# Kernel tuning notes

Measured on AMD Instinct MI355X. Metric: run time of the kernel, lower is better.

Reference implementation:

```python
import jax, jax.numpy as jnp
import numpy as np

B, N, IN, E, OUT = 4, 128, 256, 128, 128
EPS = 1e-5
NEG = -1.0e9


def _ln(x, s, o):
    m = x.mean(-1, keepdims=True)
    v = ((x - m) ** 2).mean(-1, keepdims=True)
    return s * jax.lax.rsqrt(v + EPS) * (x - m) + o


def setup_inputs() -> dict:
    key = jax.random.key(0)
    ks = jax.random.split(key, 30)

    def w(k, i, o):
        return (jax.random.normal(k, (i, o), jnp.float32) / np.sqrt(i)).astype(jnp.float32)

    z_dense = jax.random.normal(ks[0], (B, N, IN), jnp.float32)
    e_dense = jax.random.normal(ks[1], (B, N, N, E), jnp.float32)
    graph_fts = jax.random.normal(ks[2], (B, IN // 2), jnp.float32)
    lengths = jax.random.randint(ks[3], (B,), N // 2, N + 1)
    mask = jnp.arange(N)[None, :] < lengths[:, None]  # (B,N) bool
    adj = jax.random.uniform(ks[4], (B, N, N)) < 0.3
    adj = (adj | jnp.eye(N, dtype=bool)[None]) & mask[:, :, None] & mask[:, None, :]
    return dict(
        z_dense=z_dense, e_dense=e_dense, graph_fts=graph_fts, mask=mask, adj_mat=adj,
        Wt1=w(ks[5], IN, 8), Wt2=w(ks[6], IN, 8), Wt3=w(ks[7], IN, 8),
        We1=w(ks[8], E, 8), We2=w(ks[9], E, 8), We3=w(ks[10], E, 8),
        Wg=w(ks[11], IN // 2, 8),
        Wm1=w(ks[12], IN, OUT), Wm2=w(ks[13], IN, OUT), Wme=w(ks[14], E, OUT), Wmg=w(ks[15], E, OUT),
        ln1_s=jnp.ones((OUT,), jnp.float32), ln1_o=jnp.zeros((OUT,), jnp.float32),
        Wmlp1=w(ks[16], OUT, OUT),
        ln2_s=jnp.ones((OUT,), jnp.float32), ln2_o=jnp.zeros((OUT,), jnp.float32),
        Wmlp2=w(ks[17], OUT, OUT),
        WU1=w(ks[18], IN, OUT), WU2=w(ks[19], OUT, OUT), WU3=w(ks[20], 8, OUT),
        lnf_s=jnp.ones((OUT,), jnp.float32), lnf_o=jnp.zeros((OUT,), jnp.float32),
    )


def reference(z_dense, e_dense, graph_fts, mask, adj_mat,
              Wt1, Wt2, Wt3, We1, We2, We3, Wg,
              Wm1, Wm2, Wme, Wmg,
              ln1_s, ln1_o, Wmlp1, ln2_s, ln2_o, Wmlp2,
              WU1, WU2, WU3, lnf_s, lnf_o):
    mN = mask[..., None]  # (B,N,1)
    # --- triplet messages ---
    tri_1 = jnp.where(mN, z_dense @ Wt1, 0.0)  # (B,N,8)
    tri_2 = jnp.where(mN, z_dense @ Wt2, 0.0)
    tri_3 = jnp.where(mN, z_dense @ Wt3, 0.0)
    tri_e1 = e_dense @ We1  # (B,N,N,8)
    tri_e2 = e_dense @ We2
    tri_e3 = e_dense @ We3
    tri_g = graph_fts @ Wg  # (B,8)
    # (B,N,N,N,8) 7-way broadcast sum (axes: b, i, j, k)
    tri = (tri_1[:, :, None, None, :] + tri_2[:, None, :, None, :] + tri_3[:, None, None, :, :]
           + tri_e1[:, :, :, None, :] + tri_e2[:, :, None, :, :] + tri_e3[:, None, :, :, :]
           + tri_g[:, None, None, None, :])
    msk_tri = mask[:, None, None, :] | mask[:, None, :, None] | mask[:, :, None, None]
    tri = jnp.where(msk_tri[..., None], tri, NEG)
    tri_pooled = tri.max(axis=1)  # (B,N,N,8) -- max over first node axis
    tri_msgs = jax.nn.relu(tri_pooled @ WU3)  # (B,N,N,OUT)

    # --- pairwise messages ---
    msg_1 = jnp.where(mN, z_dense @ Wm1, 0.0)  # (B,N,OUT)
    msg_2 = jnp.where(mN, z_dense @ Wm2, 0.0)
    msg_e = jnp.where(adj_mat[..., None], e_dense @ Wme, 0.0)  # (B,N,N,OUT)
    msg_g = graph_fts @ Wmg  # (B,OUT)
    msgs = msg_1[:, None, :, :] + msg_2[:, :, None, :] + msg_e + msg_g[:, None, None, :]
    # M[-1]: [LN, ReLU, Linear] x2
    x = jax.nn.relu(_ln(msgs, ln1_s, ln1_o)) @ Wmlp1
    x = jax.nn.relu(_ln(x, ln2_s, ln2_o)) @ Wmlp2
    msgs = jnp.where(adj_mat[..., None], x, NEG).max(axis=1)  # (B,N,OUT)

    ret = _ln(z_dense @ WU1 + msgs @ WU2, lnf_s, lnf_o)  # (B,N,OUT)
    return ret, msgs, tri_msgs
```

## Files before the change

### kernel.cpp

```cpp
#include <hip/hip_runtime.h>

#define BN   4
#define NN   128
#define INF  256
#define EF   128
#define OUTF 128
#define EPSF 1e-5f
#define NEGF -998244352.0f

typedef __attribute__((ext_vector_type(8))) short short8;
typedef __attribute__((ext_vector_type(4))) float f32x4;

#define MFMA16(a, b, c) __builtin_amdgcn_mfma_f32_16x16x32_bf16(a, b, c, 0, 0, 0)

__device__ __forceinline__ unsigned short f2bf(float f) {
    unsigned u = __float_as_uint(f);
    u += 0x7fffu + ((u >> 16) & 1u);
    return (unsigned short)(u >> 16);
}
__device__ __forceinline__ unsigned pack2(float a, float b) {
    return (unsigned)f2bf(a) | ((unsigned)f2bf(b) << 16);
}

constexpr size_t TRI1 = 0;
constexpr size_t TRI2 = 4096;
constexpr size_t TRI3 = 8192;
constexpr size_t MSG1 = 12288;
constexpr size_t MSG2 = 77824;
constexpr size_t ZWU1 = 143360;
constexpr size_t TRIG = 208896;
constexpr size_t MSGG = 209920;
constexpr size_t E1T  = 210944;
constexpr size_t E2T  = 735232;
constexpr size_t E3N  = 1259520;
constexpr size_t PREPF = 1914880;

constexpr int W1T_OFF  = 0;
constexpr int W2T_OFF  = 16384;
constexpr int WMET_OFF = 32768;

constexpr size_t O_RET = 0;
constexpr size_t O_MSG = 65536;
constexpr size_t O_TRI = 131072;

__device__ __forceinline__ int detect_int(const void* mask) {
    const unsigned char* m = (const unsigned char*)mask;
    return (m[1] | m[2] | m[3]) == 0 ? 1 : 0;
}
__device__ __forceinline__ bool rdbool(const void* p, size_t idx, int isInt) {
    if (isInt) return ((const int*)p)[idx] != 0;
    return ((const unsigned char*)p)[idx] != 0;
}

__device__ __forceinline__ void stage_h(const unsigned short* __restrict__ prep, int offU,
                                        unsigned short* Wl, int w, int lane)
{
    const char* g = (const char*)(prep + offU) + w * 4096 + lane * 16;
    char* l = (char*)Wl + w * 4096;
    #pragma unroll
    for (int r = 0; r < 4; r++) {
        __builtin_amdgcn_global_load_lds(
            (const __attribute__((address_space(1))) void*)(g + r * 1024),
            (__attribute__((address_space(3))) void*)(l + r * 1024),
            16, 0, 0);
    }
}

__global__ __launch_bounds__(256, 4) void k_pre(
    const float* __restrict__ z, const float* __restrict__ e, const void* __restrict__ mask,
    const float* __restrict__ Wt1, const float* __restrict__ Wt2, const float* __restrict__ Wt3,
    const float* __restrict__ Wm1, const float* __restrict__ Wm2, const float* __restrict__ WU1,
    const float* __restrict__ g, const float* __restrict__ Wg, const float* __restrict__ Wmg,
    const float* __restrict__ W1, const float* __restrict__ W2, const float* __restrict__ Wme,
    const float* __restrict__ We1, const float* __restrict__ We2, const float* __restrict__ We3,
    float* __restrict__ ws, unsigned short* __restrict__ prep)
{
    int bx = blockIdx.x, tid = threadIdx.x;
    __shared__ __align__(16) unsigned char smem[128 * 136 * 2];

    if (bx < 512) {
        unsigned short* Ab = (unsigned short*)smem;
        int bi = bx;
        int b = bi >> 7, i = bi & 127;
        int lane = tid & 63, w = tid >> 6, q = lane >> 4, n = lane & 15;
        {
            int half = lane >> 5, c4 = (lane & 31) * 4;
            #pragma unroll
            for (int it = 0; it < 16; it++) {
                int row = 32 * w + 2 * it + half;
                float4 v = *(const float4*)(e + (size_t)bi * 16384 + (size_t)row * 128 + c4);
                unsigned* dst = (unsigned*)&Ab[row * 136 + c4];
                dst[0] = pack2(v.x, v.y);
                dst[1] = pack2(v.z, v.w);
            }
        }
        float t1v;
        {
            int c = lane & 7, kk = lane >> 3;
            const float* zr = z + (size_t)bi * INF;
            float s = 0.f;
            #pragma unroll
            for (int m = 0; m < 32; m++) s = fmaf(zr[kk * 32 + m], Wt1[(kk * 32 + m) * 8 + c], s);
            s += __shfl_xor(s, 8, 64);
            s += __shfl_xor(s, 16, 64);
            s += __shfl_xor(s, 32, 64);
            int isInt = detect_int(mask);
            t1v = rdbool(mask, bi, isInt) ? s : 0.f;
        }
        short8 bfrag[4][2];
        {
            #pragma unroll
            for (int t = 0; t < 2; t++) {
                int col = 16 * t + n;
                const float* Wsel = (col < 8) ? We1 : (col < 16 ? We2 : We3);
                int csel = col & 7;
                float mval = (col < 24) ? 1.f : 0.f;
                #pragma unroll
                for (int ks = 0; ks < 4; ks++) {
                    union { short8 s; unsigned short u[8]; } tmp;
                    #pragma unroll
                    for (int jj = 0; jj < 8; jj++) {
                        int k = ks * 32 + q * 8 + jj;
                        tmp.u[jj] = f2bf(Wsel[k * 8 + csel] * mval);
                    }
                    bfrag[ks][t] = tmp.s;
                }
            }
        }
        __builtin_amdgcn_wave_barrier();

        f32x4 ac2[2][2];
        #pragma unroll
        for (int rt = 0; rt < 2; rt++)
            #pragma unroll
            for (int t = 0; t < 2; t++) ac2[rt][t] = 0.f;
        #pragma unroll
        for (int ks = 0; ks < 4; ks++) {
            int k0 = ks * 32 + q * 8;
            short8 a0 = *(const short8*)&Ab[(32 * w + n) * 136 + k0];
            short8 a1 = *(const short8*)&Ab[(32 * w + 16 + n) * 136 + k0];
            #pragma unroll
            for (int t = 0; t < 2; t++) {
                ac2[0][t] = MFMA16(a0, bfrag[ks][t], ac2[0][t]);
                ac2[1][t] = MFMA16(a1, bfrag[ks][t], ac2[1][t]);
            }
        }
        #pragma unroll
        for (int rt = 0; rt < 2; rt++)
            #pragma unroll
            for (int reg = 0; reg < 4; reg++) {
                int row = 32 * w + 16 * rt + 4 * q + reg;
                float v0 = ac2[rt][0][reg];
                if (n < 8) ws[E1T + ((size_t)(b * 128 + row) * 128 + i) * 8 + n] = v0 + t1v;
                else       ws[E2T + ((size_t)(b * 128 + row) * 128 + i) * 8 + (n - 8)] = v0;
                if (n < 8) ws[E3N + ((size_t)bi * 128 + row) * 8 + n] = ac2[rt][1][reg];
            }
        return;
    }
    if (bx < 1024) {
        int bn = bx - 512;
        int isInt = detect_int(mask);
        float* zr = (float*)smem;
        zr[tid] = z[(size_t)bn * INF + tid];
        __syncthreads();
        float mk = rdbool(mask, bn, isInt) ? 1.f : 0.f;
        for (int idx = tid; idx < 408; idx += 256) {
            const float* W; int c; size_t dst; int width; bool msk;
            if (idx < 8)        { W = Wt1; c = idx;       dst = TRI1 + (size_t)bn * 8;   width = 8;   msk = true;  }
            else if (idx < 16)  { W = Wt2; c = idx - 8;   dst = TRI2 + (size_t)bn * 8;   width = 8;   msk = true;  }
            else if (idx < 24)  { W = Wt3; c = idx - 16;  dst = TRI3 + (size_t)bn * 8;   width = 8;   msk = true;  }
            else if (idx < 152) { W = Wm1; c = idx - 24;  dst = MSG1 + (size_t)bn * 128; width = 128; msk = true;  }
            else if (idx < 280) { W = Wm2; c = idx - 152; dst = MSG2 + (size_t)bn * 128; width = 128; msk = true;  }
            else                { W = WU1; c = idx - 280; dst = ZWU1 + (size_t)bn * 128; width = 128; msk = false; }
            float a0 = 0.f, a1 = 0.f;
            #pragma unroll 8
            for (int k = 0; k < INF; k += 2) {
                a0 += zr[k] * W[k * width + c];
                a1 += zr[k + 1] * W[(k + 1) * width + c];
            }
            float acc = a0 + a1;
            ws[dst + c] = msk ? acc * mk : acc;
        }
        return;
    }
    if (bx < 1028) {
        int b = bx - 1024;
        float* gr = (float*)smem;
        if (tid < 128) gr[tid] = g[b * 128 + tid];
        __syncthreads();
        if (tid < 8) {
            float a = 0.f;
            for (int k = 0; k < 128; k++) a += gr[k] * Wg[k * 8 + tid];
            ws[TRIG + b * 8 + tid] = a;
        } else if (tid >= 128) {
            int c = tid - 128;
            float a = 0.f;
            for (int k = 0; k < 128; k++) a += gr[k] * Wmg[k * 128 + c];
            ws[MSGG + b * 128 + c] = a;
        }
        return;
    }
    {
        int idx = (bx - 1028) * 256 + tid;
        const float* W = (idx < 16384) ? W1 : (idx < 32768 ? W2 : Wme);
        int local = idx & 16383;
        int f = local >> 3, jj = local & 7;
        int lane = f & 63, fg = f >> 6;
        int t = fg & 7, ks = fg >> 3;
        int n = lane & 15, q = lane >> 4;
        int row = 16 * t + n;
        int k = ks * 32 + q * 8 + jj;
        prep[idx] = f2bf(W[k * 128 + row]);
    }
}

#define PAIR_GEMM_H(HS) do {                                                   \
    _Pragma("unroll")                                                          \
    for (int ls = 0; ls < 2; ls++) {                                           \
        int kf = (2 * (HS) + ls) * 32 + q * 8;                                 \
        short8 a0 = *(const short8*)&Ab[(32 * w + n) * 136 + kf];              \
        short8 a1 = *(const short8*)&Ab[(32 * w + 16 + n) * 136 + kf];         \
        _Pragma("unroll")                                                      \
        for (int t = 0; t < 8; t++) {                                          \
            short8 bt = *(const short8*)&Wl[((ls * 8 + t) * 64 + lane) * 8];   \
            acc[0][t] = MFMA16(a0, bt, acc[0][t]);                             \
            acc[1][t] = MFMA16(a1, bt, acc[1][t]);                             \
        }                                                                      \
    }                                                                          \
} while (0)

__global__ __launch_bounds__(256, 3) void k_main(
    const float* __restrict__ e, const void* __restrict__ mask, const void* __restrict__ adj,
    const float* __restrict__ ln1s, const float* __restrict__ ln1o,
    const float* __restrict__ ln2s, const float* __restrict__ ln2o,
    const unsigned short* __restrict__ prep, const float* __restrict__ WU3,
    const float* __restrict__ WU2, const float* __restrict__ lnfs, const float* __restrict__ lnfo,
    float* __restrict__ ws, float* __restrict__ out)
{
    int bx = blockIdx.x, tid = threadIdx.x;
    __shared__ __align__(16) unsigned char smem[53248];
    int lane = tid & 63, w = tid >> 6, q = lane >> 4, n = lane & 15;
    int isInt = detect_int(mask);

    if (bx < 256) {
        int g = bx;
        int j0 = ((g >> 3) & 7) * 16, k0 = (g & 7) * 16, b = g >> 6;
        int wi = w >> 1, wc = w & 1;
        int tj = lane >> 3, tk = lane & 7;
        int col4 = (tid & 31) * 4, rowgrp = tid >> 5;

        int lenb;
        {
            unsigned long long m0 = __ballot(rdbool(mask, (size_t)b * 128 + lane, isInt));
            unsigned long long m1 = __ballot(rdbool(mask, (size_t)b * 128 + 64 + lane, isInt));
            lenb = __popcll(m0) + __popcll(m1);
        }
        bool needU = (j0 + 15 >= lenb) && (k0 + 15 >= lenb);

        float* Pb = (float*)smem + w * 1152;
        float* Qb = Pb + 576;

        f32x4 aM[2][2];
        #pragma unroll
        for (int jj = 0; jj < 2; jj++)
            #pragma unroll
            for (int kk = 0; kk < 2; kk++) aM[jj][kk] = NEGF;

        if (!needU) {
            for (int ch = 0; ch < 8; ch++) {
                int ibase = wi * 64 + ch * 8;
                #pragma unroll
                for (int r = 0; r < 2; r++) {
                    int f = r * 64 + lane;
                    int jr = f >> 3, ii = f & 7;
                    f32x4 pv = *(const f32x4*)(ws + E1T + (size_t)(b * 128 + j0 + jr) * 1024 + (ibase + ii) * 8 + wc * 4);
                    f32x4 qv = *(const f32x4*)(ws + E2T + (size_t)(b * 128 + k0 + jr) * 1024 + (ibase + ii) * 8 + wc * 4);
                    *(f32x4*)(Pb + jr * 36 + ii * 4) = pv;
                    *(f32x4*)(Qb + jr * 36 + ii * 4) = qv;
                }
                __builtin_amdgcn_wave_barrier();
                #pragma unroll
                for (int ii = 0; ii < 8; ii++) {
                    f32x4 p0 = *(const f32x4*)(Pb + tj * 36 + ii * 4);
                    f32x4 p1 = *(const f32x4*)(Pb + (tj + 8) * 36 + ii * 4);
                    f32x4 q0 = *(const f32x4*)(Qb + tk * 36 + ii * 4);
                    f32x4 q1 = *(const f32x4*)(Qb + (tk + 8) * 36 + ii * 4);
                    aM[0][0] = __builtin_elementwise_max(aM[0][0], p0 + q0);
                    aM[0][1] = __builtin_elementwise_max(aM[0][1], p0 + q1);
                    aM[1][0] = __builtin_elementwise_max(aM[1][0], p1 + q0);
                    aM[1][1] = __builtin_elementwise_max(aM[1][1], p1 + q1);
                }
            }
        } else {
            f32x4 aU[2][2];
            #pragma unroll
            for (int jj = 0; jj < 2; jj++)
                #pragma unroll
                for (int kk = 0; kk < 2; kk++) aU[jj][kk] = NEGF;
            unsigned long long mball = __ballot(rdbool(mask, (size_t)b * 128 + wi * 64 + lane, isInt));
            for (int ch = 0; ch < 8; ch++) {
                int ibase = wi * 64 + ch * 8;
                #pragma unroll
                for (int r = 0; r < 2; r++) {
                    int f = r * 64 + lane;
                    int jr = f >> 3, ii = f & 7;
                    f32x4 pv = *(const f32x4*)(ws + E1T + (size_t)(b * 128 + j0 + jr) * 1024 + (ibase + ii) * 8 + wc * 4);
                    f32x4 qv = *(const f32x4*)(ws + E2T + (size_t)(b * 128 + k0 + jr) * 1024 + (ibase + ii) * 8 + wc * 4);
                    *(f32x4*)(Pb + jr * 36 + ii * 4) = pv;
                    *(f32x4*)(Qb + jr * 36 + ii * 4) = qv;
                }
                __builtin_amdgcn_wave_barrier();
                #pragma unroll
                for (int ii = 0; ii < 8; ii++) {
                    f32x4 p0 = *(const f32x4*)(Pb + tj * 36 + ii * 4);
                    f32x4 p1 = *(const f32x4*)(Pb + (tj + 8) * 36 + ii * 4);
                    f32x4 q0 = *(const f32x4*)(Qb + tk * 36 + ii * 4);
                    f32x4 q1 = *(const f32x4*)(Qb + (tk + 8) * 36 + ii * 4);
                    f32x4 v00 = p0 + q0, v01 = p0 + q1, v10 = p1 + q0, v11 = p1 + q1;
                    if ((mball >> (ch * 8 + ii)) & 1) {
                        aM[0][0] = __builtin_elementwise_max(aM[0][0], v00);
                        aM[0][1] = __builtin_elementwise_max(aM[0][1], v01);
                        aM[1][0] = __builtin_elementwise_max(aM[1][0], v10);
                        aM[1][1] = __builtin_elementwise_max(aM[1][1], v11);
                    } else {
                        aU[0][0] = __builtin_elementwise_max(aU[0][0], v00);
                        aU[0][1] = __builtin_elementwise_max(aU[0][1], v01);
                        aU[1][0] = __builtin_elementwise_max(aU[1][0], v10);
                        aU[1][1] = __builtin_elementwise_max(aU[1][1], v11);
                    }
                }
            }
            bool mj[2], mk2[2];
            mj[0]  = (j0 + tj)     < lenb;
            mj[1]  = (j0 + tj + 8) < lenb;
            mk2[0] = (k0 + tk)     < lenb;
            mk2[1] = (k0 + tk + 8) < lenb;
            #pragma unroll
            for (int jj = 0; jj < 2; jj++)
                #pragma unroll
                for (int kk = 0; kk < 2; kk++)
                    if (mj[jj] | mk2[kk])
                        aM[jj][kk] = __builtin_elementwise_max(aM[jj][kk], aU[jj][kk]);
        }
        __syncthreads();
        float* pooled = (float*)smem;
        float4 wvr[8];
        #pragma unroll
        for (int c = 0; c < 8; c++) wvr[c] = *(const float4*)(WU3 + c * 128 + col4);

        if (wi == 0) {
            #pragma unroll
            for (int jj = 0; jj < 2; jj++)
                #pragma unroll
                for (int kk = 0; kk < 2; kk++) {
                    int p = (tj + 8 * jj) * 16 + (tk + 8 * kk);
                    #pragma unroll
                    for (int cc = 0; cc < 4; cc++)
                        pooled[(wc * 4 + cc) * 260 + p] = aM[jj][kk][cc];
                }
        }
        __syncthreads();
        if (wi == 1) {
            const float* tg = ws + TRIG + (size_t)b * 8 + wc * 4;
            #pragma unroll
            for (int jj = 0; jj < 2; jj++)
                #pragma unroll
                for (int kk = 0; kk < 2; kk++) {
                    int jv = j0 + tj + 8 * jj, kv = k0 + tk + 8 * kk;
                    const float* t2 = ws + TRI2 + (size_t)(b * 128 + jv) * 8 + wc * 4;
                    const float* t3 = ws + TRI3 + (size_t)(b * 128 + kv) * 8 + wc * 4;
                    const float* e3 = ws + E3N + ((size_t)(b * 128 + jv) * 128 + kv) * 8 + wc * 4;
                    int p = (tj + 8 * jj) * 16 + (tk + 8 * kk);
                    #pragma unroll
                    for (int cc = 0; cc < 4; cc++) {
                        int idx = (wc * 4 + cc) * 260 + p;
                        pooled[idx] = fmaxf(pooled[idx], aM[jj][kk][cc]) + t2[cc] + t3[cc] + e3[cc] + tg[cc];
                    }
                }
        }
        __syncthreads();
        #pragma unroll
        for (int pass = 0; pass < 32; pass++) {
            int p = pass * 8 + rowgrp;
            float4 s = { 0.f, 0.f, 0.f, 0.f };
            #pragma unroll
            for (int c = 0; c < 8; c++) {
                float pv = pooled[c * 260 + p];
                s.x += pv * wvr[c].x; s.y += pv * wvr[c].y;
                s.z += pv * wvr[c].z; s.w += pv * wvr[c].w;
            }
            s.x = fmaxf(s.x, 0.f); s.y = fmaxf(s.y, 0.f);
            s.z = fmaxf(s.z, 0.f); s.w = fmaxf(s.w, 0.f);
            int pj = p >> 4, pk = p & 15;
            *(float4*)(out + O_TRI + ((size_t)(b * 128 + j0 + pj) * 128 + (k0 + pk)) * 128 + col4) = s;
        }
        return;
    }

    unsigned short* Ab = (unsigned short*)smem;
    float* pw = (float*)(smem + 34816);
    unsigned short* Wl = (unsigned short*)(smem + 36864);
    float* mrowL = (float*)(smem + 36864);
    float* partL = mrowL + 128;
    float* redL  = partL + 256;
    int bj = bx - 256;
    int b = bj >> 7, j = bj & 127;

    int lenb;
    {
        unsigned long long m0 = __ballot(rdbool(mask, (size_t)b * 128 + lane, isInt));
        unsigned long long m1 = __ballot(rdbool(mask, (size_t)b * 128 + 64 + lane, isInt));
        lenb = __popcll(m0) + __popcll(m1);
    }
    bool live = (j < lenb);

    if (live) {
        bool waveActive = (32 * w) < lenb;

        stage_h(prep, WMET_OFF, Wl, w, lane);
        if (waveActive) {
            int half = lane >> 5, c4 = (lane & 31) * 4;
            #pragma unroll
            for (int it = 0; it < 16; it++) {
                int row = 32 * w + 2 * it + half;
                float4 v = *(const float4*)(e + (((size_t)b * 128 + row) * 128 + j) * 128 + c4);
                unsigned* dst = (unsigned*)&Ab[row * 136 + c4];
                dst[0] = pack2(v.x, v.y);
                dst[1] = pack2(v.z, v.w);
            }
        }
        __syncthreads();

        float colmax[8];
        #pragma unroll
        for (int t = 0; t < 8; t++) colmax[t] = NEGF;
        float adjm[2][4];
        f32x4 acc[2][8];

        #pragma unroll
        for (int rt = 0; rt < 2; rt++)
            #pragma unroll
            for (int t = 0; t < 8; t++) acc[rt][t] = 0.f;
        if (waveActive) PAIR_GEMM_H(0);
        __syncthreads();
        stage_h(prep, WMET_OFF + 8192, Wl, w, lane);
        __syncthreads();
        if (waveActive) PAIR_GEMM_H(1);
        __syncthreads();
        stage_h(prep, W1T_OFF, Wl, w, lane);

        if (waveActive) {
            float msum[8];
            #pragma unroll
            for (int t = 0; t < 8; t++)
                msum[t] = ws[MSG1 + (size_t)bj * 128 + 16 * t + n] + ws[MSGG + (size_t)b * 128 + 16 * t + n];
            float rs[2][4], rss[2][4];
            #pragma unroll
            for (int rt = 0; rt < 2; rt++)
                #pragma unroll
                for (int reg = 0; reg < 4; reg++) {
                    int row = 32 * w + 16 * rt + 4 * q + reg;
                    bool av = rdbool(adj, ((size_t)b * 128 + row) * 128 + j, isInt);
                    adjm[rt][reg] = av ? 1.f : 0.f;
                    float s = 0.f, ssq = 0.f;
                    #pragma unroll
                    for (int t = 0; t < 8; t++) {
                        float v = acc[rt][t][reg] * adjm[rt][reg]
                                + ws[MSG2 + ((size_t)b * 128 + row) * 128 + 16 * t + n] + msum[t];
                        acc[rt][t][reg] = v;
                        s += v; ssq += v * v;
                    }
                    rs[rt][reg] = s; rss[rt][reg] = ssq;
                }
            #pragma unroll
            for (int d = 1; d < 16; d <<= 1) {
                #pragma unroll
                for (int rt = 0; rt < 2; rt++)
                    #pragma unroll
                    for (int reg = 0; reg < 4; reg++) {
                        rs[rt][reg]  += __shfl_xor(rs[rt][reg], d, 64);
                        rss[rt][reg] += __shfl_xor(rss[rt][reg], d, 64);
                    }
            }
            float s1v[8], o1v[8];
            #pragma unroll
            for (int t = 0; t < 8; t++) { s1v[t] = ln1s[16 * t + n]; o1v[t] = ln1o[16 * t + n]; }
            #pragma unroll
            for (int rt = 0; rt < 2; rt++)
                #pragma unroll
                for (int reg = 0; reg < 4; reg++) {
                    float mu = rs[rt][reg] * (1.f / 128);
                    float inv = rsqrtf(rss[rt][reg] * (1.f / 128) - mu * mu + EPSF);
                    int row = 32 * w + 16 * rt + 4 * q + reg;
                    #pragma unroll
                    for (int t = 0; t < 8; t++) {
                        float v = fmaxf(s1v[t] * inv * (acc[rt][t][reg] - mu) + o1v[t], 0.f);
                        Ab[row * 136 + 16 * t + n] = f2bf(v);
                    }
                }
        }
        __syncthreads();

        #pragma unroll
        for (int rt = 0; rt < 2; rt++)
            #pragma unroll
            for (int t = 0; t < 8; t++) acc[rt][t] = 0.f;
        if (waveActive) PAIR_GEMM_H(0);
        __syncthreads();
        stage_h(prep, W1T_OFF + 8192, Wl, w, lane);
        __syncthreads();
        if (waveActive) PAIR_GEMM_H(1);
        __syncthreads();
        stage_h(prep, W2T_OFF, Wl, w, lane);

        if (waveActive) {
            float rs[2][4], rss[2][4];
            #pragma unroll
            for (int rt = 0; rt < 2; rt++)
                #pragma unroll
                for (int reg = 0; reg < 4; reg++) {
                    float s = 0.f, ssq = 0.f;
                    #pragma unroll
                    for (int t = 0; t < 8; t++) { float v = acc[rt][t][reg]; s += v; ssq += v * v; }
                    rs[rt][reg] = s; rss[rt][reg] = ssq;
                }
            #pragma unroll
            for (int d = 1; d < 16; d <<= 1) {
                #pragma unroll
                for (int rt = 0; rt < 2; rt++)
                    #pragma unroll
                    for (int reg = 0; reg < 4; reg++) {
                        rs[rt][reg]  += __shfl_xor(rs[rt][reg], d, 64);
                        rss[rt][reg] += __shfl_xor(rss[rt][reg], d, 64);
                    }
            }
            float s2v[8], o2v[8];
            #pragma unroll
            for (int t = 0; t < 8; t++) { s2v[t] = ln2s[16 * t + n]; o2v[t] = ln2o[16 * t + n]; }
            #pragma unroll
            for (int rt = 0; rt < 2; rt++)
                #pragma unroll
                for (int reg = 0; reg < 4; reg++) {
                    float mu = rs[rt][reg] * (1.f / 128);
                    float inv = rsqrtf(rss[rt][reg] * (1.f / 128) - mu * mu + EPSF);
                    int row = 32 * w + 16 * rt + 4 * q + reg;
                    #pragma unroll
                    for (int t = 0; t < 8; t++) {
                        float v = fmaxf(s2v[t] * inv * (acc[rt][t][reg] - mu) + o2v[t], 0.f);
                        Ab[row * 136 + 16 * t + n] = f2bf(v);
                    }
                }
        }
        __syncthreads();

        #pragma unroll
        for (int rt = 0; rt < 2; rt++)
            #pragma unroll
            for (int t = 0; t < 8; t++) acc[rt][t] = 0.f;
        if (waveActive) PAIR_GEMM_H(0);
        __syncthreads();
        stage_h(prep, W2T_OFF + 8192, Wl, w, lane);
        __syncthreads();
        if (waveActive) {
            PAIR_GEMM_H(1);
            #pragma unroll
            for (int rt = 0; rt < 2; rt++)
                #pragma unroll
                for (int reg = 0; reg < 4; reg++) {
                    if (adjm[rt][reg] > 0.f) {
                        #pragma unroll
                        for (int t = 0; t < 8; t++) colmax[t] = fmaxf(colmax[t], acc[rt][t][reg]);
                    }
                }
        }
        #pragma unroll
        for (int t = 0; t < 8; t++) {
            colmax[t] = fmaxf(colmax[t], __shfl_xor(colmax[t], 16, 64));
            colmax[t] = fmaxf(colmax[t], __shfl_xor(colmax[t], 32, 64));
        }
        if (lane < 16) {
            #pragma unroll
            for (int t = 0; t < 8; t++) pw[w * 128 + 16 * t + lane] = colmax[t];
        }
        __syncthreads();
        if (tid < 128) {
            float mx = fmaxf(fmaxf(pw[tid], pw[128 + tid]), fmaxf(pw[256 + tid], pw[384 + tid]));
            mrowL[tid] = mx;
            out[O_MSG + (size_t)bj * 128 + tid] = mx;
        }
    } else {
        if (tid < 128) {
            mrowL[tid] = NEGF;
            out[O_MSG + (size_t)bj * 128 + tid] = NEGF;
        }
    }
    __syncthreads();

    {
        int c = tid & 127, hf = tid >> 7;
        int kb = hf * 64;
        float a0 = 0.f, a1 = 0.f;
        #pragma unroll 8
        for (int k = 0; k < 64; k += 2) {
            a0 = fmaf(mrowL[kb + k],     WU2[(size_t)(kb + k) * 128 + c],     a0);
            a1 = fmaf(mrowL[kb + k + 1], WU2[(size_t)(kb + k + 1) * 128 + c], a1);
        }
        partL[hf * 128 + c] = a0 + a1;
        __syncthreads();
        float y = ws[ZWU1 + (size_t)bj * 128 + c] + partL[c] + partL[128 + c];
        float s = y, ss = y * y;
        #pragma unroll
        for (int d = 1; d < 64; d <<= 1) { s += __shfl_xor(s, d, 64); ss += __shfl_xor(ss, d, 64); }
        if (tid == 0 || tid == 64) { redL[(tid >> 6) * 2] = s; redL[(tid >> 6) * 2 + 1] = ss; }
        __syncthreads();
        float S = redL[0] + redL[2], SS = redL[1] + redL[3];
        float m_ = S * (1.f / 128), v_ = SS * (1.f / 128) - m_ * m_;
        float r = rsqrtf(v_ + EPSF);
        if (tid < 128) out[O_RET + (size_t)bj * 128 + c] = lnfs[c] * r * (y - m_) + lnfo[c];
    }
}

extern "C" void kernel_launch(void* const* d_in, const int* in_sizes, int n_in,
                              void* d_out, int out_size, void* d_ws, size_t ws_size,
                              hipStream_t stream)
{
    const float* z    = (const float*)d_in[0];
    const float* e    = (const float*)d_in[1];
    const float* gf   = (const float*)d_in[2];
    const void*  mask = d_in[3];
    const void*  adj  = d_in[4];
    const float* Wt1 = (const float*)d_in[5];
    const float* Wt2 = (const float*)d_in[6];
    const float* Wt3 = (const float*)d_in[7];
    const float* We1 = (const float*)d_in[8];
    const float* We2 = (const float*)d_in[9];
    const float* We3 = (const float*)d_in[10];
    const float* Wg  = (const float*)d_in[11];
    const float* Wm1 = (const float*)d_in[12];
    const float* Wm2 = (const float*)d_in[13];
    const float* Wme = (const float*)d_in[14];
    const float* Wmg = (const float*)d_in[15];
    const float* ln1s = (const float*)d_in[16];
    const float* ln1o = (const float*)d_in[17];
    const float* W1   = (const float*)d_in[18];
    const float* ln2s = (const float*)d_in[19];
    const float* ln2o = (const float*)d_in[20];
    const float* W2   = (const float*)d_in[21];
    const float* WU1  = (const float*)d_in[22];
    const float* WU2  = (const float*)d_in[23];
    const float* WU3  = (const float*)d_in[24];
    const float* lnfs = (const float*)d_in[25];
    const float* lnfo = (const float*)d_in[26];
    float* out = (float*)d_out;
    float* ws  = (float*)d_ws;
    unsigned short* prep = (unsigned short*)(ws + PREPF);

    hipLaunchKernelGGL(k_pre, dim3(1220), dim3(256), 0, stream,
                       z, e, mask, Wt1, Wt2, Wt3, Wm1, Wm2, WU1, gf, Wg, Wmg,
                       W1, W2, Wme, We1, We2, We3, ws, prep);
    hipLaunchKernelGGL(k_main, dim3(768), dim3(256), 0, stream,
                       e, mask, adj, ln1s, ln1o, ln2s, ln2o, prep, WU3,
                       WU2, lnfs, lnfo, ws, out);
}
```

Baseline: 177.5 us.

## Stage bf16 transposed edge tiles in pre-kernel and DMA them into LDS

The pre-kernel already holds each edge tile converted to bf16 in LDS and now also writes it out to a workspace buffer, laid out transposed per destination node and XOR-swizzled. The main kernel then loads its A operand with global_load_lds DMA instead of reading fp32 edges and converting them. The A buffer in LDS changes from a padded 136-element row stride to an unpadded 256-byte row with an XOR swizzle to avoid bank conflicts, which frees some LDS. In exchange the pre-kernel does an extra global write of the full edge tensor in bf16.

Measured after the change: 183.4 us. 3.3% more time.

```diff
diff --git a/kernel.cpp b/kernel.cpp
--- a/kernel.cpp
+++ b/kernel.cpp
@@ -34,6 +34,7 @@
 constexpr size_t E2T  = 735232;
 constexpr size_t E3N  = 1259520;
 constexpr size_t PREPF = 1914880;
+constexpr size_t ET_F  = 1939456;
 
 constexpr int W1T_OFF  = 0;
 constexpr int W2T_OFF  = 16384;
@@ -155,6 +156,19 @@
                 else       ws[E2T + ((size_t)(b * 128 + row) * 128 + i) * 8 + (n - 8)] = v0;
                 if (n < 8) ws[E3N + ((size_t)bi * 128 + row) * 8 + n] = ac2[rt][1][reg];
             }
+        __syncthreads();
+        {
+            unsigned short* eT = (unsigned short*)(ws + ET_F);
+            int jj = tid >> 1, hf = tid & 1;
+            int xr = (i & 7) << 4;
+            char* dstb = (char*)(eT + (size_t)(b * 128 + jj) * 16384) + i * 256;
+            const char* srcb = (const char*)&Ab[jj * 136 + hf * 64];
+            #pragma unroll
+            for (int m = 0; m < 8; m++) {
+                int off = (hf * 128 + m * 16) ^ xr;
+                *(uint4*)(dstb + off) = *(const uint4*)(srcb + m * 16);
+            }
+        }
         return;
     }
     if (bx < 1024) {
@@ -215,11 +229,12 @@
 }
 
 #define PAIR_GEMM_H(HS) do {                                                   \
+    int xa = (n & 7) << 4;                                                     \
     _Pragma("unroll")                                                          \
     for (int ls = 0; ls < 2; ls++) {                                           \
-        int kf = (2 * (HS) + ls) * 32 + q * 8;                                 \
-        short8 a0 = *(const short8*)&Ab[(32 * w + n) * 136 + kf];              \
-        short8 a1 = *(const short8*)&Ab[(32 * w + 16 + n) * 136 + kf];         \
+        int kb2 = ((2 * (HS) + ls) * 32 + q * 8) * 2;                          \
+        short8 a0 = *(const short8*)((const char*)Ab + (32 * w + n) * 256 + (kb2 ^ xa));      \
+        short8 a1 = *(const short8*)((const char*)Ab + (32 * w + 16 + n) * 256 + (kb2 ^ xa)); \
         _Pragma("unroll")                                                      \
         for (int t = 0; t < 8; t++) {                                          \
             short8 bt = *(const short8*)&Wl[((ls * 8 + t) * 64 + lane) * 8];   \
@@ -230,7 +245,7 @@
 } while (0)
 
 __global__ __launch_bounds__(256, 3) void k_main(
-    const float* __restrict__ e, const void* __restrict__ mask, const void* __restrict__ adj,
+    const void* __restrict__ mask, const void* __restrict__ adj,
     const float* __restrict__ ln1s, const float* __restrict__ ln1o,
     const float* __restrict__ ln2s, const float* __restrict__ ln2o,
     const unsigned short* __restrict__ prep, const float* __restrict__ WU3,
@@ -238,7 +253,7 @@
     float* __restrict__ ws, float* __restrict__ out)
 {
     int bx = blockIdx.x, tid = threadIdx.x;
-    __shared__ __align__(16) unsigned char smem[53248];
+    __shared__ __align__(16) unsigned char smem[51200];
     int lane = tid & 63, w = tid >> 6, q = lane >> 4, n = lane & 15;
     int isInt = detect_int(mask);
 
@@ -398,9 +413,9 @@
     }
 
     unsigned short* Ab = (unsigned short*)smem;
-    float* pw = (float*)(smem + 34816);
-    unsigned short* Wl = (unsigned short*)(smem + 36864);
-    float* mrowL = (float*)(smem + 36864);
+    float* pw = (float*)(smem + 32768);
+    unsigned short* Wl = (unsigned short*)(smem + 34816);
+    float* mrowL = (float*)(smem + 34816);
     float* partL = mrowL + 128;
     float* redL  = partL + 256;
     int bj = bx - 256;
@@ -419,14 +434,15 @@
 
         stage_h(prep, WMET_OFF, Wl, w, lane);
         if (waveActive) {
-            int half = lane >> 5, c4 = (lane & 31) * 4;
-            #pragma unroll
-            for (int it = 0; it < 16; it++) {
-                int row = 32 * w + 2 * it + half;
-                float4 v = *(const float4*)(e + (((size_t)b * 128 + row) * 128 + j) * 128 + c4);
-                unsigned* dst = (unsigned*)&Ab[row * 136 + c4];
-                dst[0] = pack2(v.x, v.y);
-                dst[1] = pack2(v.z, v.w);
+            const char* gA = (const char*)((const unsigned short*)(ws + ET_F)
+                              + (size_t)(b * 128 + j) * 16384) + w * 8192 + lane * 16;
+            char* lA = (char*)Ab + w * 8192;
+            #pragma unroll
+            for (int r = 0; r < 8; r++) {
+                __builtin_amdgcn_global_load_lds(
+                    (const __attribute__((address_space(1))) void*)(gA + r * 1024),
+                    (__attribute__((address_space(3))) void*)(lA + r * 1024),
+                    16, 0, 0);
             }
         }
         __syncthreads();
@@ -492,10 +508,11 @@
                     float mu = rs[rt][reg] * (1.f / 128);
                     float inv = rsqrtf(rss[rt][reg] * (1.f / 128) - mu * mu + EPSF);
                     int row = 32 * w + 16 * rt + 4 * q + reg;
+                    int xw = (row & 7) << 4;
                     #pragma unroll
                     for (int t = 0; t < 8; t++) {
                         float v = fmaxf(s1v[t] * inv * (acc[rt][t][reg] - mu) + o1v[t], 0.f);
-                        Ab[row * 136 + 16 * t + n] = f2bf(v);
+                        *(unsigned short*)((char*)Ab + row * 256 + ((2 * (16 * t + n)) ^ xw)) = f2bf(v);
                     }
                 }
         }
@@ -544,10 +561,11 @@
                     float mu = rs[rt][reg] * (1.f / 128);
                     float inv = rsqrtf(rss[rt][reg] * (1.f / 128) - mu * mu + EPSF);
                     int row = 32 * w + 16 * rt + 4 * q + reg;
+                    int xw = (row & 7) << 4;
                     #pragma unroll
                     for (int t = 0; t < 8; t++) {
                         float v = fmaxf(s2v[t] * inv * (acc[rt][t][reg] - mu) + o2v[t], 0.f);
-                        Ab[row * 136 + 16 * t + n] = f2bf(v);
+                        *(unsigned short*)((char*)Ab + row * 256 + ((2 * (16 * t + n)) ^ xw)) = f2bf(v);
                     }
                 }
         }
@@ -659,6 +677,6 @@
                        z, e, mask, Wt1, Wt2, Wt3, Wm1, Wm2, WU1, gf, Wg, Wmg,
                        W1, W2, Wme, We1, We2, We3, ws, prep);
     hipLaunchKernelGGL(k_main, dim3(768), dim3(256), 0, stream,
-                       e, mask, adj, ln1s, ln1o, ln2s, ln2o, prep, WU3,
+                       mask, adj, ln1s, ln1o, ln2s, ln2o, prep, WU3,
                        WU2, lnfs, lnfo, ws, out);
 }
```

## Double-buffer weight staging in quarter-K chunks to overlap loads with MFMA

Applied to the files above, without the earlier changes.

Weight tiles for the three per-pair GEMMs are now staged into LDS in four K-quarter chunks, alternating between two buffers. The asynchronous global-to-LDS load of the next chunk is issued before the MFMA work on the current chunk, so the copy overlaps compute. This also drops one barrier per GEMM. The cost is smaller per-stage load batches and more dependence on barrier-implied waits to make the buffer reuse safe. Total LDS use stays the same.

After: 181.7 us. +2.4%, slower.

```diff
diff --git a/kernel.cpp b/kernel.cpp
--- a/kernel.cpp
+++ b/kernel.cpp
@@ -52,13 +52,13 @@
     return ((const unsigned char*)p)[idx] != 0;
 }
 
-__device__ __forceinline__ void stage_h(const unsigned short* __restrict__ prep, int offU,
+__device__ __forceinline__ void stage_q(const unsigned short* __restrict__ prep, int offU,
                                         unsigned short* Wl, int w, int lane)
 {
-    const char* g = (const char*)(prep + offU) + w * 4096 + lane * 16;
-    char* l = (char*)Wl + w * 4096;
+    const char* g = (const char*)(prep + offU) + w * 2048 + lane * 16;
+    char* l = (char*)Wl + w * 2048;
     #pragma unroll
-    for (int r = 0; r < 4; r++) {
+    for (int r = 0; r < 2; r++) {
         __builtin_amdgcn_global_load_lds(
             (const __attribute__((address_space(1))) void*)(g + r * 1024),
             (__attribute__((address_space(3))) void*)(l + r * 1024),
@@ -214,18 +214,15 @@
     }
 }
 
-#define PAIR_GEMM_H(HS) do {                                                   \
+#define PAIR_GEMM_S(S, WL) do {                                                \
+    int kf = (S) * 32 + q * 8;                                                 \
+    short8 a0 = *(const short8*)&Ab[(32 * w + n) * 136 + kf];                  \
+    short8 a1 = *(const short8*)&Ab[(32 * w + 16 + n) * 136 + kf];             \
     _Pragma("unroll")                                                          \
-    for (int ls = 0; ls < 2; ls++) {                                           \
-        int kf = (2 * (HS) + ls) * 32 + q * 8;                                 \
-        short8 a0 = *(const short8*)&Ab[(32 * w + n) * 136 + kf];              \
-        short8 a1 = *(const short8*)&Ab[(32 * w + 16 + n) * 136 + kf];         \
-        _Pragma("unroll")                                                      \
-        for (int t = 0; t < 8; t++) {                                          \
-            short8 bt = *(const short8*)&Wl[((ls * 8 + t) * 64 + lane) * 8];   \
-            acc[0][t] = MFMA16(a0, bt, acc[0][t]);                             \
-            acc[1][t] = MFMA16(a1, bt, acc[1][t]);                             \
-        }                                                                      \
+    for (int t = 0; t < 8; t++) {                                              \
+        short8 bt = *(const short8*)&(WL)[(t * 64 + lane) * 8];                \
+        acc[0][t] = MFMA16(a0, bt, acc[0][t]);                                 \
+        acc[1][t] = MFMA16(a1, bt, acc[1][t]);                                 \
     }                                                                          \
 } while (0)
 
@@ -399,7 +396,8 @@
 
     unsigned short* Ab = (unsigned short*)smem;
     float* pw = (float*)(smem + 34816);
-    unsigned short* Wl = (unsigned short*)(smem + 36864);
+    unsigned short* Wl0 = (unsigned short*)(smem + 36864);
+    unsigned short* Wl1 = (unsigned short*)(smem + 45056);
     float* mrowL = (float*)(smem + 36864);
     float* partL = mrowL + 128;
     float* redL  = partL + 256;
@@ -417,7 +415,7 @@
     if (live) {
         bool waveActive = (32 * w) < lenb;
 
-        stage_h(prep, WMET_OFF, Wl, w, lane);
+        stage_q(prep, WMET_OFF, Wl0, w, lane);
         if (waveActive) {
             int half = lane >> 5, c4 = (lane & 31) * 4;
             #pragma unroll
@@ -441,13 +439,17 @@
         for (int rt = 0; rt < 2; rt++)
             #pragma unroll
             for (int t = 0; t < 8; t++) acc[rt][t] = 0.f;
-        if (waveActive) PAIR_GEMM_H(0);
-        __syncthreads();
-        stage_h(prep, WMET_OFF + 8192, Wl, w, lane);
-        __syncthreads();
-        if (waveActive) PAIR_GEMM_H(1);
-        __syncthreads();
-        stage_h(prep, W1T_OFF, Wl, w, lane);
+        stage_q(prep, WMET_OFF + 4096, Wl1, w, lane);
+        if (waveActive) PAIR_GEMM_S(0, Wl0);
+        __syncthreads();
+        stage_q(prep, WMET_OFF + 8192, Wl0, w, lane);
+        if (waveActive) PAIR_GEMM_S(1, Wl1);
+        __syncthreads();
+        stage_q(prep, WMET_OFF + 12288, Wl1, w, lane);
+        if (waveActive) PAIR_GEMM_S(2, Wl0);
+        __syncthreads();
+        stage_q(prep, W1T_OFF, Wl0, w, lane);
+        if (waveActive) PAIR_GEMM_S(3, Wl1);
 
         if (waveActive) {
             float msum[8];
@@ -505,13 +507,17 @@
         for (int rt = 0; rt < 2; rt++)
             #pragma unroll
             for (int t = 0; t < 8; t++) acc[rt][t] = 0.f;
-        if (waveActive) PAIR_GEMM_H(0);
-        __syncthreads();
-        stage_h(prep, W1T_OFF + 8192, Wl, w, lane);
-        __syncthreads();
-        if (waveActive) PAIR_GEMM_H(1);
-        __syncthreads();
-        stage_h(prep, W2T_OFF, Wl, w, lane);
+        stage_q(prep, W1T_OFF + 4096, Wl1, w, lane);
+        if (waveActive) PAIR_GEMM_S(0, Wl0);
+        __syncthreads();
+        stage_q(prep, W1T_OFF + 8192, Wl0, w, lane);
+        if (waveActive) PAIR_GEMM_S(1, Wl1);
+        __syncthreads();
+        stage_q(prep, W1T_OFF + 12288, Wl1, w, lane);
+        if (waveActive) PAIR_GEMM_S(2, Wl0);
+        __syncthreads();
+        stage_q(prep, W2T_OFF, Wl0, w, lane);
+        if (waveActive) PAIR_GEMM_S(3, Wl1);
 
         if (waveActive) {
             float rs[2][4], rss[2][4];
@@ -557,12 +563,17 @@
         for (int rt = 0; rt < 2; rt++)
             #pragma unroll
             for (int t = 0; t < 8; t++) acc[rt][t] = 0.f;
-        if (waveActive) PAIR_GEMM_H(0);
-        __syncthreads();
-        stage_h(prep, W2T_OFF + 8192, Wl, w, lane);
+        stage_q(prep, W2T_OFF + 4096, Wl1, w, lane);
+        if (waveActive) PAIR_GEMM_S(0, Wl0);
+        __syncthreads();
+        stage_q(prep, W2T_OFF + 8192, Wl0, w, lane);
+        if (waveActive) PAIR_GEMM_S(1, Wl1);
+        __syncthreads();
+        stage_q(prep, W2T_OFF + 12288, Wl1, w, lane);
+        if (waveActive) PAIR_GEMM_S(2, Wl0);
         __syncthreads();
         if (waveActive) {
-            PAIR_GEMM_H(1);
+            PAIR_GEMM_S(3, Wl1);
             #pragma unroll
             for (int rt = 0; rt < 2; rt++)
                 #pragma unroll
```
